# Performance work log

Measured on AMD Instinct MI355X. Metric: run time of the kernel, lower is better.

The kernel has to match this reference:

```python
import jax, jax.numpy as jnp
import numpy as np

HEADS = 4
DIM_HEAD = 64
INNER = HEADS * DIM_HEAD  # 256
MAP_SIZE = (8, 8, 8)
DN = ('NCDHW', 'OIDHW', 'NCDHW')


def _depthwise3d(x, w):
    # x: [B,C,D,H,W], w: [C,1,3,3,3] (torch groups=C layout)
    return jax.lax.conv_general_dilated(
        x, w, window_strides=(1, 1, 1), padding='SAME',
        dimension_numbers=DN, feature_group_count=x.shape[1])


def _dws_conv(x, dw, pw):
    # depthwise 3x3x3 then pointwise 1x1x1 (pw: [out,in])
    y = _depthwise3d(x, dw)
    return jnp.einsum('bcdhw,oc->bodhw', y, pw)


def _split_heads(t):
    # 'b (dim_head heads) d h w -> b heads (d h w) dim_head'
    B, C, D, H, W = t.shape
    t = t.reshape(B, DIM_HEAD, HEADS, D * H * W)
    return t.transpose(0, 2, 3, 1)


def _merge_heads(t, D, H, W):
    # 'b heads n dim_head -> b (dim_head heads) d h w'
    B = t.shape[0]
    return t.transpose(0, 3, 1, 2).reshape(B, DIM_HEAD * HEADS, D, H, W)


def setup_inputs() -> dict:
    key = jax.random.key(0)
    ks = jax.random.split(key, 8)
    B, feat_dim, map_dim, out_dim = 2, 128, 64, 128
    D = H = W = 24
    s = 0.02
    return {
        'feat': jax.random.normal(ks[0], (B, feat_dim, D, H, W), jnp.float32),
        'smap': jax.random.normal(ks[1], (B, map_dim) + MAP_SIZE, jnp.float32),
        'feat_qv_dw': jax.random.normal(ks[2], (feat_dim, 1, 3, 3, 3), jnp.float32) * s,
        'feat_qv_pw': jax.random.normal(ks[3], (2 * INNER, feat_dim), jnp.float32) * s,
        'feat_out_dw': jax.random.normal(ks[4], (INNER, 1, 3, 3, 3), jnp.float32) * s,
        'feat_out_pw': jax.random.normal(ks[5], (out_dim, INNER), jnp.float32) * s,
        'map_qv_w': jax.random.normal(ks[6], (2 * INNER, map_dim), jnp.float32) * s,
        'map_out_w': jax.random.normal(ks[7], (map_dim, INNER), jnp.float32) * s,
    }


def reference(feat, smap, feat_qv_dw, feat_qv_pw, feat_out_dw, feat_out_pw,
              map_qv_w, map_out_w):
    B, C, D, H, W = feat.shape
    scale = DIM_HEAD ** -0.5

    # projections
    fqv = _dws_conv(feat, feat_qv_dw, feat_qv_pw)           # [B, 2*inner, D,H,W]
    feat_q, feat_v = jnp.split(fqv, 2, axis=1)
    mqv = jnp.einsum('bcdhw,oc->bodhw', smap, map_qv_w)     # [B, 2*inner, 8,8,8]
    map_q, map_v = jnp.split(mqv, 2, axis=1)

    feat_q, feat_v = _split_heads(feat_q), _split_heads(feat_v)  # [B,h,N,dh]
    map_q, map_v = _split_heads(map_q), _split_heads(map_v)      # [B,h,M,dh]

    # shared scores, dual-direction softmax
    attn = jnp.einsum('bhid,bhjd->bhij', feat_q, map_q) * scale  # [B,h,N,M]
    feat_map_attn = jax.nn.softmax(attn, axis=-1)
    map_feat_attn = jax.nn.softmax(attn, axis=-2)

    feat_out = jnp.einsum('bhij,bhjd->bhid', feat_map_attn, map_v)   # [B,h,N,dh]
    map_out = jnp.einsum('bhji,bhjd->bhid', map_feat_attn, feat_v)   # [B,h,M,dh]

    feat_out = _merge_heads(feat_out, D, H, W)
    map_out = _merge_heads(map_out, *MAP_SIZE)

    feat_out = _dws_conv(feat_out, feat_out_dw, feat_out_pw)   # [B,out_dim,D,H,W]
    map_out = jnp.einsum('bcdhw,oc->bodhw', map_out, map_out_w)  # [B,map_dim,8,8,8]
    return feat_out, map_out
```

## Files before the change

kernel.cpp:

```cpp
#include <hip/hip_runtime.h>

#define BB 2
#define CH_FEAT 128
#define HEADS 4
#define DH 64
#define INNER 256
#define NPOS 13824
#define MPOS 512
#define DSZ 24
#define JSPLIT 27
#define JCHUNK (NPOS / JSPLIT)

typedef __attribute__((ext_vector_type(8))) short bf16x8;
typedef __attribute__((ext_vector_type(4))) float f32x4;

__device__ inline unsigned short bf16_rn(float x) {
  unsigned u = __builtin_bit_cast(unsigned, x);
  u += 0x7FFF + ((u >> 16) & 1);
  return (unsigned short)(u >> 16);
}
__device__ inline unsigned pk_bf16(float a, float b) {
  return (unsigned)bf16_rn(a) | ((unsigned)bf16_rn(b) << 16);
}
__device__ inline float bf2f(unsigned short u) {
  return __builtin_bit_cast(float, (unsigned)u << 16);
}

#define GL2LDS(g, l)                                                        \
  __builtin_amdgcn_global_load_lds(                                         \
      (const __attribute__((address_space(1))) void*)(g),                   \
      (__attribute__((address_space(3))) void*)(l), 16, 0, 0)

__device__ inline bf16x8 lds_frag(const char* tile, int row, int colb) {
  return *(const bf16x8*)(tile + row * 128 + (colb ^ ((row & 7) << 4)));
}
__device__ inline bf16x8 lds_fragP(const char* tile, int row, int colb, int pitch) {
  return *(const bf16x8*)(tile + row * pitch + (colb ^ ((row & 7) << 4)));
}

__global__ __launch_bounds__(256) void k_pre(const float* __restrict__ smap,
                                             const float* __restrict__ mqv_w,
                                             unsigned short* __restrict__ mapqb,
                                             unsigned short* __restrict__ mapvTb,
                                             const float* __restrict__ feat,
                                             const float* __restrict__ fqv_dw,
                                             unsigned short* __restrict__ dwt) {
  int bid = blockIdx.x;
  int t = threadIdx.x;
  if (bid < 1024) {
    int b = bid >> 9, m = bid & 511;
    __shared__ float s[64];
    if (t < 64) s[t] = smap[(size_t)(b * 64 + t) * MPOS + m];
    __syncthreads();
#pragma unroll
    for (int half = 0; half < 2; ++half) {
      int co2 = half * 256 + t;
      const float* wr = mqv_w + (size_t)co2 * 64;
      float acc = 0.f;
#pragma unroll
      for (int c = 0; c < 64; ++c) acc += wr[c] * s[c];
      int qv = co2 >> 8, c2 = co2 & 255, head = c2 & 3, dh = c2 >> 2;
      int bh = b * HEADS + head;
      if (qv == 0)
        mapqb[((size_t)bh * MPOS + m) * 64 + dh] = bf16_rn(acc * 0.125f);
      else
        mapvTb[((size_t)bh * 64 + dh) * MPOS + m] = bf16_rn(acc);
    }
  } else {
    int tid = (bid - 1024) * 256 + t;
    int bc = tid / 1728;
    int s = tid - bc * 1728;
    int c = bc & (CH_FEAT - 1);
    int xs = (s % 3) * 8;
    int row = s / 3;
    int y = row % 24, z = row / 24;
    const float* wr = fqv_dw + c * 27;
    const float* ip = feat + (size_t)bc * NPOS;

    float w0a[9], w1a[9], w2a[9];
    int ro[9];
#pragma unroll
    for (int dz = 0; dz < 3; ++dz)
#pragma unroll
      for (int dy = 0; dy < 3; ++dy) {
        int r = dz * 3 + dy;
        int zz = z + dz - 1, yy = y + dy - 1;
        bool ok = ((unsigned)zz < 24u) && ((unsigned)yy < 24u);
        w0a[r] = ok ? wr[dz * 9 + dy * 3 + 0] : 0.f;
        w1a[r] = ok ? wr[dz * 9 + dy * 3 + 1] : 0.f;
        w2a[r] = ok ? wr[dz * 9 + dy * 3 + 2] : 0.f;
        int zc = min(max(zz, 0), 23), yc = min(max(yy, 0), 23);
        ro[r] = (zc * 24 + yc) * 24;
      }
    float4 Bv[9], Cv[9];
    float xm1[9], x8[9];
#pragma unroll
    for (int r = 0; r < 9; ++r) {
      Bv[r] = *(const float4*)(ip + ro[r] + xs);
      Cv[r] = *(const float4*)(ip + ro[r] + xs + 4);
      xm1[r] = xs ? *(ip + ro[r] + xs - 1) : 0.f;
      x8[r] = (xs < 16) ? *(ip + ro[r] + xs + 8) : 0.f;
    }
    float acc[8];
#pragma unroll
    for (int i = 0; i < 8; ++i) acc[i] = 0.f;
#pragma unroll
    for (int r = 0; r < 9; ++r) {
      float xv[10] = {xm1[r], Bv[r].x, Bv[r].y, Bv[r].z, Bv[r].w,
                      Cv[r].x, Cv[r].y, Cv[r].z, Cv[r].w, x8[r]};
#pragma unroll
      for (int i = 0; i < 8; ++i)
        acc[i] += w0a[r] * xv[i] + w1a[r] * xv[i + 1] + w2a[r] * xv[i + 2];
    }
    unsigned short* op = dwt + (size_t)bc * NPOS + row * 24 + xs;
    uint4 pv;
    pv.x = pk_bf16(acc[0], acc[1]);
    pv.y = pk_bf16(acc[2], acc[3]);
    pv.z = pk_bf16(acc[4], acc[5]);
    pv.w = pk_bf16(acc[6], acc[7]);
    *(uint4*)op = pv;
  }
}

__global__ __launch_bounds__(256) void k_pwqv_m(const unsigned short* __restrict__ dwt,
                                                const float* __restrict__ pw,
                                                unsigned short* __restrict__ fqb,
                                                unsigned short* __restrict__ fvTb) {
  __shared__ __align__(16) char sW[16384];
  __shared__ __align__(16) char sR[32768];
  __shared__ __align__(16) char sB[32768];
  int t = threadIdx.x, wave = t >> 6, lane = t & 63, g = lane >> 4, c = lane & 15;
  int n0 = blockIdx.x * 128, ti = blockIdx.y, b = blockIdx.z;
  int qv = ti >> 2, head = ti & 3, bh = b * 4 + head;

  {
    int r = t >> 2, ks = (t & 3) * 32;
    int co = qv * 256 + r * 4 + head;
    const float* wp = pw + (size_t)co * 128 + ks;
    unsigned pkv[16];
#pragma unroll
    for (int i = 0; i < 8; ++i) {
      float4 v = *(const float4*)(wp + i * 4);
      pkv[2 * i] = pk_bf16(v.x, v.y);
      pkv[2 * i + 1] = pk_bf16(v.z, v.w);
    }
#pragma unroll
    for (int u = 0; u < 4; ++u) {
      int colb = (ks * 2 + u * 16) ^ ((r & 7) << 4);
      *(uint4*)(sW + r * 256 + colb) = *(uint4*)&pkv[u * 4];
    }
  }
  const char* Bgc = (const char*)(dwt + (size_t)b * CH_FEAT * NPOS);
#pragma unroll
  for (int p = 0; p < 8; ++p) {
    int oo = p * 4096 + t * 16;
    int k = oo >> 8, col = oo & 255;
    GL2LDS(Bgc + (size_t)k * (NPOS * 2) + n0 * 2 + col, sR + oo);
  }
  __syncthreads();

  {
    const unsigned short* R16 = (const unsigned short*)sR;
#pragma unroll
    for (int it = 0; it < 8; ++it) {
      int cid = it * 256 + t;
      int n = cid & 127, kc16 = (cid >> 7) & 15;
      unsigned short v[8];
#pragma unroll
      for (int j = 0; j < 8; ++j) v[j] = R16[(kc16 * 8 + j) * 128 + n];
      unsigned u4[4];
#pragma unroll
      for (int i = 0; i < 4; ++i)
        u4[i] = (unsigned)v[2 * i] | ((unsigned)v[2 * i + 1] << 16);
      *(uint4*)(sB + n * 256 + ((kc16 * 16) ^ ((n & 7) << 4))) = *(uint4*)&u4[0];
    }
  }
  __syncthreads();

  f32x4 acc[4][2];
#pragma unroll
  for (int ct = 0; ct < 4; ++ct)
#pragma unroll
    for (int jf = 0; jf < 2; ++jf) acc[ct][jf] = (f32x4){0.f, 0.f, 0.f, 0.f};
  int nw = wave * 32;
#pragma unroll
  for (int kc = 0; kc < 4; ++kc) {
    bf16x8 bq[2];
#pragma unroll
    for (int jf = 0; jf < 2; ++jf)
      bq[jf] = lds_fragP(sB, nw + jf * 16 + c, kc * 64 + g * 16, 256);
#pragma unroll
    for (int ct = 0; ct < 4; ++ct) {
      bf16x8 a = lds_fragP(sW, ct * 16 + c, kc * 64 + g * 16, 256);
#pragma unroll
      for (int jf = 0; jf < 2; ++jf)
        acc[ct][jf] = __builtin_amdgcn_mfma_f32_16x16x32_bf16(a, bq[jf], acc[ct][jf], 0, 0, 0);
    }
  }
  __syncthreads();

  char* dmp = sR;
#pragma unroll
  for (int ct = 0; ct < 4; ++ct)
#pragma unroll
    for (int jf = 0; jf < 2; ++jf) {
      int n = nw + jf * 16 + c;
      uint2 wv;
      wv.x = pk_bf16(acc[ct][jf][0], acc[ct][jf][1]);
      wv.y = pk_bf16(acc[ct][jf][2], acc[ct][jf][3]);
      *(uint2*)(dmp + n * 144 + (ct * 16 + 4 * g) * 2) = wv;
    }
  __syncthreads();

  if (qv == 0) {
    int nr = t >> 1, seg = t & 1;
    const char* src = dmp + nr * 144 + seg * 64;
    unsigned short* dst = fqb + ((size_t)bh * NPOS + n0 + nr) * 64 + seg * 32;
#pragma unroll
    for (int i = 0; i < 4; ++i)
      *(uint4*)(dst + i * 8) = *(const uint4*)(src + i * 16);
  } else {
#pragma unroll
    for (int it = 0; it < 2; ++it) {
      int idx = it * 256 + t;
      int dh = idx >> 3, nseg = (idx & 7) * 16;
      unsigned pkv[8];
#pragma unroll
      for (int i = 0; i < 8; ++i) {
        unsigned short lo = *(const unsigned short*)(dmp + (nseg + 2 * i) * 144 + dh * 2);
        unsigned short hi = *(const unsigned short*)(dmp + (nseg + 2 * i + 1) * 144 + dh * 2);
        pkv[i] = (unsigned)lo | ((unsigned)hi << 16);
      }
      unsigned short* dst = fvTb + ((size_t)bh * 64 + dh) * NPOS + n0 + nseg;
      *(uint4*)(dst) = *(uint4*)&pkv[0];
      *(uint4*)(dst + 8) = *(uint4*)&pkv[4];
    }
  }
}

__global__ __launch_bounds__(512, 4) void k_attn(const unsigned short* __restrict__ fqb,
                                                 const unsigned short* __restrict__ fvTb,
                                                 const unsigned short* __restrict__ mapqb,
                                                 const unsigned short* __restrict__ mapvTb,
                                                 unsigned short* __restrict__ F,
                                                 float* __restrict__ Gc,
                                                 float* __restrict__ Gl) {
  __shared__ __align__(16) char sAll[70656];
  char* sPool = sAll;
  unsigned (*sP)[2][16][36] = (unsigned (*)[2][16][36])(sAll + 32768);
  float (*sL)[2][16] = (float (*)[2][16])(sAll + 32768 + 36864);
  int bid = blockIdx.x;
  int t = threadIdx.x, wave = t >> 6, lane = t & 63, g = lane >> 4, c = lane & 15;

  if (bid < 432) {
    int jblk = bid % 54, bh = bid / 54;
    int j0 = jblk * 256 + wave * 32;

    const char* Kg = (const char*)(mapqb + (size_t)bh * MPOS * 64);
    const char* Vg = (const char*)(mapvTb + (size_t)bh * 64 * MPOS);

    const unsigned short* fqp = fqb + ((size_t)bh * NPOS + j0 + c) * 64 + 8 * g;
    bf16x8 bq00 = *(const bf16x8*)(fqp);
    bf16x8 bq01 = *(const bf16x8*)(fqp + 32);
    bf16x8 bq10 = *(const bf16x8*)(fqp + 16 * 64);
    bf16x8 bq11 = *(const bf16x8*)(fqp + 16 * 64 + 32);

    f32x4 o[2][4];
#pragma unroll
    for (int jf = 0; jf < 2; ++jf)
#pragma unroll
      for (int dt = 0; dt < 4; ++dt) o[jf][dt] = (f32x4){0.f, 0.f, 0.f, 0.f};
    float ls0 = 0.f, ls1 = 0.f;

    {
      int oo = t * 16;
      int row = oo >> 7, col = (oo & 127) ^ (((oo >> 7) & 7) << 4);
      GL2LDS(Kg + (size_t)row * 128 + col, sPool + oo);
      GL2LDS(Vg + (size_t)row * 1024 + col, sPool + 16384 + oo);
    }
    __syncthreads();

    for (int ic = 0; ic < 8; ++ic) {
      const char* Kt = sPool + (ic & 1) * 8192;
      const char* Vt = sPool + 16384 + (ic & 1) * 8192;
      if (ic < 7) {
        int ibase = (ic + 1) * 64;
        int bsel = ((ic + 1) & 1) * 8192;
        int oo = t * 16;
        int row = oo >> 7, col = (oo & 127) ^ (((oo >> 7) & 7) << 4);
        GL2LDS(Kg + (size_t)(ibase + row) * 128 + col, sPool + bsel + oo);
        GL2LDS(Vg + (size_t)row * 1024 + ibase * 2 + col, sPool + 16384 + bsel + oo);
      }
#pragma unroll
      for (int ti = 0; ti < 4; ++ti) {
        bf16x8 a0 = lds_frag(Kt, ti * 16 + c, 16 * g);
        bf16x8 a1 = lds_frag(Kt, ti * 16 + c, 64 + 16 * g);
        f32x4 s0 = {0.f, 0.f, 0.f, 0.f}, s1 = {0.f, 0.f, 0.f, 0.f};
        s0 = __builtin_amdgcn_mfma_f32_16x16x32_bf16(a0, bq00, s0, 0, 0, 0);
        s0 = __builtin_amdgcn_mfma_f32_16x16x32_bf16(a1, bq01, s0, 0, 0, 0);
        s1 = __builtin_amdgcn_mfma_f32_16x16x32_bf16(a0, bq10, s1, 0, 0, 0);
        s1 = __builtin_amdgcn_mfma_f32_16x16x32_bf16(a1, bq11, s1, 0, 0, 0);
        float p0 = __expf(s0[0]), p1 = __expf(s0[1]), p2 = __expf(s0[2]), p3 = __expf(s0[3]);
        ls0 += (p0 + p1) + (p2 + p3);
        sP[wave][0][c][ti * 8 + 2 * g] = pk_bf16(p0, p1);
        sP[wave][0][c][ti * 8 + 2 * g + 1] = pk_bf16(p2, p3);
        float q0 = __expf(s1[0]), q1 = __expf(s1[1]), q2 = __expf(s1[2]), q3 = __expf(s1[3]);
        ls1 += (q0 + q1) + (q2 + q3);
        sP[wave][1][c][ti * 8 + 2 * g] = pk_bf16(q0, q1);
        sP[wave][1][c][ti * 8 + 2 * g + 1] = pk_bf16(q2, q3);
      }
#pragma unroll
      for (int ks = 0; ks < 2; ++ks) {
        bf16x8 ap0 = *(const bf16x8*)&sP[wave][0][c][ks * 16 + 4 * g];
        bf16x8 ap1 = *(const bf16x8*)&sP[wave][1][c][ks * 16 + 4 * g];
#pragma unroll
        for (int dt = 0; dt < 4; ++dt) {
          bf16x8 bv = lds_frag(Vt, dt * 16 + c, ks * 64 + 16 * g);
          o[0][dt] = __builtin_amdgcn_mfma_f32_16x16x32_bf16(ap0, bv, o[0][dt], 0, 0, 0);
          o[1][dt] = __builtin_amdgcn_mfma_f32_16x16x32_bf16(ap1, bv, o[1][dt], 0, 0, 0);
        }
      }
      __syncthreads();
    }

    ls0 += __shfl_xor(ls0, 16); ls0 += __shfl_xor(ls0, 32);
    ls1 += __shfl_xor(ls1, 16); ls1 += __shfl_xor(ls1, 32);
    if (g == 0) { sL[wave][0][c] = 1.f / ls0; sL[wave][1][c] = 1.f / ls1; }
#pragma unroll
    for (int jf = 0; jf < 2; ++jf) {
      float rl0 = sL[wave][jf][4 * g + 0], rl1 = sL[wave][jf][4 * g + 1];
      float rl2 = sL[wave][jf][4 * g + 2], rl3 = sL[wave][jf][4 * g + 3];
#pragma unroll
      for (int dt = 0; dt < 4; ++dt) {
        uint2 wv;
        wv.x = pk_bf16(o[jf][dt][0] * rl0, o[jf][dt][1] * rl1);
        wv.y = pk_bf16(o[jf][dt][2] * rl2, o[jf][dt][3] * rl3);
        *(uint2*)(sAll + (dt * 16 + c) * 544 + (wave * 32 + jf * 16 + 4 * g) * 2) = wv;
      }
    }
    __syncthreads();
    {
      int ch = t >> 3, seg = t & 7;
      int b = bh >> 2, head = bh & 3;
      unsigned short* dst = F + ((size_t)b * INNER + head * 64 + ch) * NPOS +
                            jblk * 256 + seg * 32;
      const char* src = sAll + ch * 544 + seg * 64;
#pragma unroll
      for (int i = 0; i < 4; ++i)
        *(uint4*)(dst + i * 8) = *(const uint4*)(src + i * 16);
    }
  } else {
    int cid = bid - 432;
    int bh = cid & 7, iblk = (cid >> 3) & 1, chunk = cid >> 4;
    char* sQ = sPool;
    char* sV = sPool + 16384;
    int i0 = iblk * 256 + wave * 32;
    int jb = chunk * JCHUNK;

    const char* Qg = (const char*)(fqb + (size_t)bh * NPOS * 64);
    const char* Vg = (const char*)(fvTb + (size_t)bh * 64 * NPOS);

    const unsigned short* kp = mapqb + ((size_t)bh * MPOS + i0 + c) * 64 + 8 * g;
    bf16x8 bm00 = *(const bf16x8*)(kp);
    bf16x8 bm01 = *(const bf16x8*)(kp + 32);
    bf16x8 bm10 = *(const bf16x8*)(kp + 16 * 64);
    bf16x8 bm11 = *(const bf16x8*)(kp + 16 * 64 + 32);

    f32x4 o[2][4];
#pragma unroll
    for (int f = 0; f < 2; ++f)
#pragma unroll
      for (int dt = 0; dt < 4; ++dt) o[f][dt] = (f32x4){0.f, 0.f, 0.f, 0.f};
    float lc0 = 0.f, lc1 = 0.f;

    {
      int oo = t * 16;
      int row = oo >> 7, col = (oo & 127) ^ (((oo >> 7) & 7) << 4);
      GL2LDS(Qg + (size_t)(jb + row) * 128 + col, sQ + oo);
      GL2LDS(Vg + (size_t)row * (NPOS * 2) + jb * 2 + col, sV + oo);
    }
    __syncthreads();

    for (int jc = 0; jc < JCHUNK / 64; ++jc) {
      const char* Qt = sQ + (jc & 1) * 8192;
      const char* Vt = sV + (jc & 1) * 8192;
      if (jc < JCHUNK / 64 - 1) {
        int jbase = jb + (jc + 1) * 64;
        int bsel = ((jc + 1) & 1) * 8192;
        int oo = t * 16;
        int row = oo >> 7, col = (oo & 127) ^ (((oo >> 7) & 7) << 4);
        GL2LDS(Qg + (size_t)(jbase + row) * 128 + col, sQ + bsel + oo);
        GL2LDS(Vg + (size_t)row * (NPOS * 2) + jbase * 2 + col, sV + bsel + oo);
      }
#pragma unroll
      for (int tj = 0; tj < 4; ++tj) {
        bf16x8 a0 = lds_frag(Qt, tj * 16 + c, 16 * g);
        bf16x8 a1 = lds_frag(Qt, tj * 16 + c, 64 + 16 * g);
        f32x4 s0 = {0.f, 0.f, 0.f, 0.f}, s1 = {0.f, 0.f, 0.f, 0.f};
        s0 = __builtin_amdgcn_mfma_f32_16x16x32_bf16(a0, bm00, s0, 0, 0, 0);
        s0 = __builtin_amdgcn_mfma_f32_16x16x32_bf16(a1, bm01, s0, 0, 0, 0);
        s1 = __builtin_amdgcn_mfma_f32_16x16x32_bf16(a0, bm10, s1, 0, 0, 0);
        s1 = __builtin_amdgcn_mfma_f32_16x16x32_bf16(a1, bm11, s1, 0, 0, 0);
        float p0 = __expf(s0[0]), p1 = __expf(s0[1]), p2 = __expf(s0[2]), p3 = __expf(s0[3]);
        lc0 += (p0 + p1) + (p2 + p3);
        sP[wave][0][c][tj * 8 + 2 * g] = pk_bf16(p0, p1);
        sP[wave][0][c][tj * 8 + 2 * g + 1] = pk_bf16(p2, p3);
        float q0 = __expf(s1[0]), q1 = __expf(s1[1]), q2 = __expf(s1[2]), q3 = __expf(s1[3]);
        lc1 += (q0 + q1) + (q2 + q3);
        sP[wave][1][c][tj * 8 + 2 * g] = pk_bf16(q0, q1);
        sP[wave][1][c][tj * 8 + 2 * g + 1] = pk_bf16(q2, q3);
      }
#pragma unroll
      for (int ks = 0; ks < 2; ++ks) {
        bf16x8 ap0 = *(const bf16x8*)&sP[wave][0][c][ks * 16 + 4 * g];
        bf16x8 ap1 = *(const bf16x8*)&sP[wave][1][c][ks * 16 + 4 * g];
#pragma unroll
        for (int dt = 0; dt < 4; ++dt) {
          bf16x8 bv = lds_frag(Vt, dt * 16 + c, ks * 64 + 16 * g);
          o[0][dt] = __builtin_amdgcn_mfma_f32_16x16x32_bf16(ap0, bv, o[0][dt], 0, 0, 0);
          o[1][dt] = __builtin_amdgcn_mfma_f32_16x16x32_bf16(ap1, bv, o[1][dt], 0, 0, 0);
        }
      }
      __syncthreads();
    }

    lc0 += __shfl_xor(lc0, 16); lc0 += __shfl_xor(lc0, 32);
    lc1 += __shfl_xor(lc1, 16); lc1 += __shfl_xor(lc1, 32);
    int gi = chunk * 8 + bh;
    if (g == 0) {
      Gl[(size_t)gi * MPOS + i0 + c] = lc0;
      Gl[(size_t)gi * MPOS + i0 + 16 + c] = lc1;
    }
    float* gp = Gc + ((size_t)gi * MPOS + i0) * 64;
#pragma unroll
    for (int f = 0; f < 2; ++f)
#pragma unroll
      for (int dt = 0; dt < 4; ++dt)
#pragma unroll
        for (int r = 0; r < 4; ++r)
          gp[(size_t)(f * 16 + 4 * g + r) * 64 + dt * 16 + c] = o[f][dt][r];
  }
}

__global__ __launch_bounds__(256) void k_post(const unsigned short* __restrict__ F,
                                              const float* __restrict__ fout_dw,
                                              unsigned short* __restrict__ dwt2,
                                              const float* __restrict__ Gc,
                                              const float* __restrict__ Gl,
                                              const float* __restrict__ mow,
                                              float* __restrict__ out2) {
  int bid = blockIdx.x;
  int t = threadIdx.x;
  if (bid < 3456) {
    int tid = bid * 256 + t;
    int bc = tid / 1728;
    int s = tid - bc * 1728;
    int c = bc & (INNER - 1), b = bc / INNER;
    int cm = (c & 63) * 4 + (c >> 6);
    int xs = (s % 3) * 8;
    int row = s / 3;
    int y = row % 24, z = row / 24;
    const float* wr = fout_dw + cm * 27;
    const unsigned short* ip = F + (size_t)bc * NPOS;

    float w0a[9], w1a[9], w2a[9];
    int ro[9];
#pragma unroll
    for (int dz = 0; dz < 3; ++dz)
#pragma unroll
      for (int dy = 0; dy < 3; ++dy) {
        int r = dz * 3 + dy;
        int zz = z + dz - 1, yy = y + dy - 1;
        bool ok = ((unsigned)zz < 24u) && ((unsigned)yy < 24u);
        w0a[r] = ok ? wr[dz * 9 + dy * 3 + 0] : 0.f;
        w1a[r] = ok ? wr[dz * 9 + dy * 3 + 1] : 0.f;
        w2a[r] = ok ? wr[dz * 9 + dy * 3 + 2] : 0.f;
        int zc = min(max(zz, 0), 23), yc = min(max(yy, 0), 23);
        ro[r] = (zc * 24 + yc) * 24;
      }
    uint2 Bu[9], Cu[9];
    unsigned short m1[9], p8[9];
#pragma unroll
    for (int r = 0; r < 9; ++r) {
      Bu[r] = *(const uint2*)(ip + ro[r] + xs);
      Cu[r] = *(const uint2*)(ip + ro[r] + xs + 4);
      m1[r] = xs ? ip[ro[r] + xs - 1] : 0;
      p8[r] = (xs < 16) ? ip[ro[r] + xs + 8] : 0;
    }
    float acc[8];
#pragma unroll
    for (int i = 0; i < 8; ++i) acc[i] = 0.f;
#pragma unroll
    for (int r = 0; r < 9; ++r) {
      float xv[10];
      xv[0] = bf2f(m1[r]);
      xv[1] = __builtin_bit_cast(float, (Bu[r].x & 0xFFFFu) << 16);
      xv[2] = __builtin_bit_cast(float, Bu[r].x & 0xFFFF0000u);
      xv[3] = __builtin_bit_cast(float, (Bu[r].y & 0xFFFFu) << 16);
      xv[4] = __builtin_bit_cast(float, Bu[r].y & 0xFFFF0000u);
      xv[5] = __builtin_bit_cast(float, (Cu[r].x & 0xFFFFu) << 16);
      xv[6] = __builtin_bit_cast(float, Cu[r].x & 0xFFFF0000u);
      xv[7] = __builtin_bit_cast(float, (Cu[r].y & 0xFFFFu) << 16);
      xv[8] = __builtin_bit_cast(float, Cu[r].y & 0xFFFF0000u);
      xv[9] = bf2f(p8[r]);
#pragma unroll
      for (int i = 0; i < 8; ++i)
        acc[i] += w0a[r] * xv[i] + w1a[r] * xv[i + 1] + w2a[r] * xv[i + 2];
    }
    unsigned short* op = dwt2 + ((size_t)b * INNER + cm) * NPOS + row * 24 + xs;
    uint4 pv;
    pv.x = pk_bf16(acc[0], acc[1]);
    pv.y = pk_bf16(acc[2], acc[3]);
    pv.z = pk_bf16(acc[4], acc[5]);
    pv.w = pk_bf16(acc[6], acc[7]);
    *(uint4*)op = pv;
  } else {
    int mi = bid - 3456;
    int m = mi & 511, b = mi >> 9;
    __shared__ float sMA[256];
    __shared__ float sL2[4];
    if (t < 4) {
      float l = 0.f;
#pragma unroll 4
      for (int ch = 0; ch < JSPLIT; ++ch)
        l += Gl[(size_t)(ch * 8 + b * 4 + t) * MPOS + m];
      sL2[t] = 1.f / l;
    }
    __syncthreads();
    {
      int head = t & 3, dh = t >> 2;
      int bh = b * 4 + head;
      float a = 0.f;
#pragma unroll 4
      for (int ch = 0; ch < JSPLIT; ++ch)
        a += Gc[((size_t)(ch * 8 + bh) * MPOS + m) * 64 + dh];
      sMA[t] = a * sL2[head];
    }
    __syncthreads();
    if (t < 64) {
      const float* wr = mow + t * 256;
      float acc = 0.f;
#pragma unroll 4
      for (int c = 0; c < 256; ++c) acc += wr[c] * sMA[c];
      out2[((size_t)b * 64 + t) * MPOS + m] = acc;
    }
  }
}

__global__ __launch_bounds__(256) void k_pwout_m(const unsigned short* __restrict__ dwo,
                                                 const float* __restrict__ pw,
                                                 float* __restrict__ out1) {
  __shared__ __align__(16) char sW[32768];
  __shared__ __align__(16) char sB[32768];
  __shared__ __align__(16) char sR[16384];
  int t = threadIdx.x, wave = t >> 6, lane = t & 63, g = lane >> 4, c = lane & 15;
  int n0 = blockIdx.x * 128, ti = blockIdx.y, b = blockIdx.z;

  {
    int r = t >> 2, ks = (t & 3) * 64;
    const float* wp = pw + (size_t)(ti * 64 + r) * 256 + ks;
    unsigned pkv[32];
#pragma unroll
    for (int i = 0; i < 16; ++i) {
      float4 v = *(const float4*)(wp + i * 4);
      pkv[2 * i] = pk_bf16(v.x, v.y);
      pkv[2 * i + 1] = pk_bf16(v.z, v.w);
    }
#pragma unroll
    for (int u = 0; u < 8; ++u) {
      int colb = (ks * 2 + u * 16) ^ ((r & 7) << 4);
      *(uint4*)(sW + r * 512 + colb) = *(uint4*)&pkv[u * 4];
    }
  }

  f32x4 acc[4][2];
#pragma unroll
  for (int ct = 0; ct < 4; ++ct)
#pragma unroll
    for (int jf = 0; jf < 2; ++jf) acc[ct][jf] = (f32x4){0.f, 0.f, 0.f, 0.f};
  int nw = wave * 32;
  const char* Bgc = (const char*)(dwo + (size_t)b * INNER * NPOS);
  const unsigned short* R16 = (const unsigned short*)sR;

  for (int kh = 0; kh < 2; ++kh) {
#pragma unroll
    for (int q = 0; q < 2; ++q) {
#pragma unroll
      for (int p = 0; p < 4; ++p) {
        int oo = p * 4096 + t * 16;
        int kl = oo >> 8, col = oo & 255;
        GL2LDS(Bgc + (size_t)(kh * 128 + q * 64 + kl) * (NPOS * 2) + n0 * 2 + col,
               sR + oo);
      }
      __syncthreads();
#pragma unroll
      for (int it = 0; it < 4; ++it) {
        int cid = it * 256 + t;
        int n = cid & 127, kcl = (cid >> 7) & 7;
        unsigned short v[8];
#pragma unroll
        for (int j = 0; j < 8; ++j) v[j] = R16[(kcl * 8 + j) * 128 + n];
        unsigned u4[4];
#pragma unroll
        for (int i = 0; i < 4; ++i)
          u4[i] = (unsigned)v[2 * i] | ((unsigned)v[2 * i + 1] << 16);
        int kc16 = q * 8 + kcl;
        *(uint4*)(sB + n * 256 + ((kc16 * 16) ^ ((n & 7) << 4))) = *(uint4*)&u4[0];
      }
      __syncthreads();
    }
#pragma unroll
    for (int kc = 0; kc < 4; ++kc) {
      bf16x8 bq[2];
#pragma unroll
      for (int jf = 0; jf < 2; ++jf)
        bq[jf] = lds_fragP(sB, nw + jf * 16 + c, kc * 64 + g * 16, 256);
#pragma unroll
      for (int ct = 0; ct < 4; ++ct) {
        bf16x8 a = lds_fragP(sW, ct * 16 + c, (kh * 4 + kc) * 64 + g * 16, 512);
#pragma unroll
        for (int jf = 0; jf < 2; ++jf)
          acc[ct][jf] = __builtin_amdgcn_mfma_f32_16x16x32_bf16(a, bq[jf], acc[ct][jf], 0, 0, 0);
      }
    }
    __syncthreads();
  }
#pragma unroll
  for (int ct = 0; ct < 4; ++ct)
#pragma unroll
    for (int jf = 0; jf < 2; ++jf) {
      int n = n0 + nw + jf * 16 + c;
#pragma unroll
      for (int r = 0; r < 4; ++r) {
        int co = ti * 64 + ct * 16 + 4 * g + r;
        out1[((size_t)b * 128 + co) * NPOS + n] = acc[ct][jf][r];
      }
    }
}

extern "C" void kernel_launch(void* const* d_in, const int* in_sizes, int n_in,
                              void* d_out, int out_size, void* d_ws, size_t ws_size,
                              hipStream_t stream) {
  const float* feat = (const float*)d_in[0];
  const float* smap = (const float*)d_in[1];
  const float* fqv_dw = (const float*)d_in[2];
  const float* fqv_pw = (const float*)d_in[3];
  const float* fout_dw = (const float*)d_in[4];
  const float* fout_pw = (const float*)d_in[5];
  const float* mqv_w = (const float*)d_in[6];
  const float* mout_w = (const float*)d_in[7];

  float* out = (float*)d_out;
  float* out1 = out;
  float* out2 = out + (size_t)BB * 128 * NPOS;

  const size_t QV = (size_t)BB * HEADS * NPOS * DH;
  const size_t MQV = (size_t)BB * HEADS * MPOS * DH;
  float* ws = (float*)d_ws;
  unsigned short* F = (unsigned short*)ws;
  unsigned short* fqb = (unsigned short*)(ws + QV);
  unsigned short* fvTb = fqb + QV;
  unsigned short* mapqb = fvTb + QV;
  unsigned short* mapvTb = mapqb + MQV;
  float* Gc = (float*)(mapvTb + MQV);
  float* Gl = Gc + (size_t)JSPLIT * 8 * MPOS * 64;

  unsigned short* dwt = (unsigned short*)out1;
  unsigned short* dwt2 = fqb;

  k_pre<<<dim3(1024 + BB * CH_FEAT * 1728 / 256), dim3(256), 0, stream>>>(
      smap, mqv_w, mapqb, mapvTb, feat, fqv_dw, dwt);
  k_pwqv_m<<<dim3(NPOS / 128, 8, BB), dim3(256), 0, stream>>>(dwt, fqv_pw, fqb, fvTb);
  k_attn<<<dim3(432 + 8 * 2 * JSPLIT), dim3(512), 0, stream>>>(
      fqb, fvTb, mapqb, mapvTb, F, Gc, Gl);
  k_post<<<dim3(BB * INNER * 1728 / 256 + BB * MPOS), dim3(256), 0, stream>>>(
      F, fout_dw, dwt2, Gc, Gl, mout_w, out2);
  k_pwout_m<<<dim3(NPOS / 128, 2, BB), dim3(256), 0, stream>>>(dwt2, fout_pw, out1);
}
```

Measured before the change: 177.3 us.

## Fold log2e into map-Q scale, interleave score/PV stages, add MFMA priority

Pre-multiplies the map query scale by log2(e) so the softmax numerators can use the native exp2 instruction instead of expf. Restructures the inner loop to compute scores and apply PV per half-chunk, halving the per-wave P staging buffer and shrinking LDS use so more blocks can reside per CU. Wraps MFMA groups in s_setprio to favour matrix issue. Risks extra LDS hazards between the halves and slightly altered scheduling.

```diff
diff --git a/kernel.cpp b/kernel.cpp
--- a/kernel.cpp
+++ b/kernel.cpp
@@ -10,6 +10,7 @@
 #define DSZ 24
 #define JSPLIT 27
 #define JCHUNK (NPOS / JSPLIT)
+#define QSCALE (0.125f * 1.44269504088896340736f)
 
 typedef __attribute__((ext_vector_type(8))) short bf16x8;
 typedef __attribute__((ext_vector_type(4))) float f32x4;
@@ -62,7 +63,7 @@
       int qv = co2 >> 8, c2 = co2 & 255, head = c2 & 3, dh = c2 >> 2;
       int bh = b * HEADS + head;
       if (qv == 0)
-        mapqb[((size_t)bh * MPOS + m) * 64 + dh] = bf16_rn(acc * 0.125f);
+        mapqb[((size_t)bh * MPOS + m) * 64 + dh] = bf16_rn(acc * QSCALE);
       else
         mapvTb[((size_t)bh * 64 + dh) * MPOS + m] = bf16_rn(acc);
     }
@@ -245,10 +246,10 @@
                                                  unsigned short* __restrict__ F,
                                                  float* __restrict__ Gc,
                                                  float* __restrict__ Gl) {
-  __shared__ __align__(16) char sAll[70656];
+  __shared__ __align__(16) char sAll[52224];
   char* sPool = sAll;
-  unsigned (*sP)[2][16][36] = (unsigned (*)[2][16][36])(sAll + 32768);
-  float (*sL)[2][16] = (float (*)[2][16])(sAll + 32768 + 36864);
+  unsigned (*sP)[2][16][18] = (unsigned (*)[2][16][18])(sAll + 32768);
+  float (*sL)[2][16] = (float (*)[2][16])(sAll + 32768 + 18432);
   int bid = blockIdx.x;
   int t = threadIdx.x, wave = t >> 6, lane = t & 63, g = lane >> 4, c = lane & 15;
 
@@ -292,33 +293,40 @@
         GL2LDS(Vg + (size_t)row * 1024 + ibase * 2 + col, sPool + 16384 + bsel + oo);
       }
 #pragma unroll
-      for (int ti = 0; ti < 4; ++ti) {
-        bf16x8 a0 = lds_frag(Kt, ti * 16 + c, 16 * g);
-        bf16x8 a1 = lds_frag(Kt, ti * 16 + c, 64 + 16 * g);
-        f32x4 s0 = {0.f, 0.f, 0.f, 0.f}, s1 = {0.f, 0.f, 0.f, 0.f};
-        s0 = __builtin_amdgcn_mfma_f32_16x16x32_bf16(a0, bq00, s0, 0, 0, 0);
-        s0 = __builtin_amdgcn_mfma_f32_16x16x32_bf16(a1, bq01, s0, 0, 0, 0);
-        s1 = __builtin_amdgcn_mfma_f32_16x16x32_bf16(a0, bq10, s1, 0, 0, 0);
-        s1 = __builtin_amdgcn_mfma_f32_16x16x32_bf16(a1, bq11, s1, 0, 0, 0);
-        float p0 = __expf(s0[0]), p1 = __expf(s0[1]), p2 = __expf(s0[2]), p3 = __expf(s0[3]);
-        ls0 += (p0 + p1) + (p2 + p3);
-        sP[wave][0][c][ti * 8 + 2 * g] = pk_bf16(p0, p1);
-        sP[wave][0][c][ti * 8 + 2 * g + 1] = pk_bf16(p2, p3);
-        float q0 = __expf(s1[0]), q1 = __expf(s1[1]), q2 = __expf(s1[2]), q3 = __expf(s1[3]);
-        ls1 += (q0 + q1) + (q2 + q3);
-        sP[wave][1][c][ti * 8 + 2 * g] = pk_bf16(q0, q1);
-        sP[wave][1][c][ti * 8 + 2 * g + 1] = pk_bf16(q2, q3);
-      }
-#pragma unroll
       for (int ks = 0; ks < 2; ++ks) {
-        bf16x8 ap0 = *(const bf16x8*)&sP[wave][0][c][ks * 16 + 4 * g];
-        bf16x8 ap1 = *(const bf16x8*)&sP[wave][1][c][ks * 16 + 4 * g];
+#pragma unroll
+        for (int tt = 0; tt < 2; ++tt) {
+          int ti = ks * 2 + tt;
+          bf16x8 a0 = lds_frag(Kt, ti * 16 + c, 16 * g);
+          bf16x8 a1 = lds_frag(Kt, ti * 16 + c, 64 + 16 * g);
+          f32x4 s0 = {0.f, 0.f, 0.f, 0.f}, s1 = {0.f, 0.f, 0.f, 0.f};
+          __builtin_amdgcn_s_setprio(1);
+          s0 = __builtin_amdgcn_mfma_f32_16x16x32_bf16(a0, bq00, s0, 0, 0, 0);
+          s0 = __builtin_amdgcn_mfma_f32_16x16x32_bf16(a1, bq01, s0, 0, 0, 0);
+          s1 = __builtin_amdgcn_mfma_f32_16x16x32_bf16(a0, bq10, s1, 0, 0, 0);
+          s1 = __builtin_amdgcn_mfma_f32_16x16x32_bf16(a1, bq11, s1, 0, 0, 0);
+          __builtin_amdgcn_s_setprio(0);
+          float p0 = __builtin_amdgcn_exp2f(s0[0]), p1 = __builtin_amdgcn_exp2f(s0[1]);
+          float p2 = __builtin_amdgcn_exp2f(s0[2]), p3 = __builtin_amdgcn_exp2f(s0[3]);
+          ls0 += (p0 + p1) + (p2 + p3);
+          sP[wave][0][c][tt * 8 + 2 * g] = pk_bf16(p0, p1);
+          sP[wave][0][c][tt * 8 + 2 * g + 1] = pk_bf16(p2, p3);
+          float q0 = __builtin_amdgcn_exp2f(s1[0]), q1 = __builtin_amdgcn_exp2f(s1[1]);
+          float q2 = __builtin_amdgcn_exp2f(s1[2]), q3 = __builtin_amdgcn_exp2f(s1[3]);
+          ls1 += (q0 + q1) + (q2 + q3);
+          sP[wave][1][c][tt * 8 + 2 * g] = pk_bf16(q0, q1);
+          sP[wave][1][c][tt * 8 + 2 * g + 1] = pk_bf16(q2, q3);
+        }
+        bf16x8 ap0 = *(const bf16x8*)&sP[wave][0][c][4 * g];
+        bf16x8 ap1 = *(const bf16x8*)&sP[wave][1][c][4 * g];
+        __builtin_amdgcn_s_setprio(1);
 #pragma unroll
         for (int dt = 0; dt < 4; ++dt) {
           bf16x8 bv = lds_frag(Vt, dt * 16 + c, ks * 64 + 16 * g);
           o[0][dt] = __builtin_amdgcn_mfma_f32_16x16x32_bf16(ap0, bv, o[0][dt], 0, 0, 0);
           o[1][dt] = __builtin_amdgcn_mfma_f32_16x16x32_bf16(ap1, bv, o[1][dt], 0, 0, 0);
         }
+        __builtin_amdgcn_s_setprio(0);
       }
       __syncthreads();
     }
@@ -393,33 +401,40 @@
         GL2LDS(Vg + (size_t)row * (NPOS * 2) + jbase * 2 + col, sV + bsel + oo);
       }
 #pragma unroll
-      for (int tj = 0; tj < 4; ++tj) {
-        bf16x8 a0 = lds_frag(Qt, tj * 16 + c, 16 * g);
-        bf16x8 a1 = lds_frag(Qt, tj * 16 + c, 64 + 16 * g);
-        f32x4 s0 = {0.f, 0.f, 0.f, 0.f}, s1 = {0.f, 0.f, 0.f, 0.f};
-        s0 = __builtin_amdgcn_mfma_f32_16x16x32_bf16(a0, bm00, s0, 0, 0, 0);
-        s0 = __builtin_amdgcn_mfma_f32_16x16x32_bf16(a1, bm01, s0, 0, 0, 0);
-        s1 = __builtin_amdgcn_mfma_f32_16x16x32_bf16(a0, bm10, s1, 0, 0, 0);
-        s1 = __builtin_amdgcn_mfma_f32_16x16x32_bf16(a1, bm11, s1, 0, 0, 0);
-        float p0 = __expf(s0[0]), p1 = __expf(s0[1]), p2 = __expf(s0[2]), p3 = __expf(s0[3]);
-        lc0 += (p0 + p1) + (p2 + p3);
-        sP[wave][0][c][tj * 8 + 2 * g] = pk_bf16(p0, p1);
-        sP[wave][0][c][tj * 8 + 2 * g + 1] = pk_bf16(p2, p3);
-        float q0 = __expf(s1[0]), q1 = __expf(s1[1]), q2 = __expf(s1[2]), q3 = __expf(s1[3]);
-        lc1 += (q0 + q1) + (q2 + q3);
-        sP[wave][1][c][tj * 8 + 2 * g] = pk_bf16(q0, q1);
-        sP[wave][1][c][tj * 8 + 2 * g + 1] = pk_bf16(q2, q3);
-      }
-#pragma unroll
       for (int ks = 0; ks < 2; ++ks) {
-        bf16x8 ap0 = *(const bf16x8*)&sP[wave][0][c][ks * 16 + 4 * g];
-        bf16x8 ap1 = *(const bf16x8*)&sP[wave][1][c][ks * 16 + 4 * g];
+#pragma unroll
+        for (int tt = 0; tt < 2; ++tt) {
+          int tj = ks * 2 + tt;
+          bf16x8 a0 = lds_frag(Qt, tj * 16 + c, 16 * g);
+          bf16x8 a1 = lds_frag(Qt, tj * 16 + c, 64 + 16 * g);
+          f32x4 s0 = {0.f, 0.f, 0.f, 0.f}, s1 = {0.f, 0.f, 0.f, 0.f};
+          __builtin_amdgcn_s_setprio(1);
+          s0 = __builtin_amdgcn_mfma_f32_16x16x32_bf16(a0, bm00, s0, 0, 0, 0);
+          s0 = __builtin_amdgcn_mfma_f32_16x16x32_bf16(a1, bm01, s0, 0, 0, 0);
+          s1 = __builtin_amdgcn_mfma_f32_16x16x32_bf16(a0, bm10, s1, 0, 0, 0);
+          s1 = __builtin_amdgcn_mfma_f32_16x16x32_bf16(a1, bm11, s1, 0, 0, 0);
+          __builtin_amdgcn_s_setprio(0);
+          float p0 = __builtin_amdgcn_exp2f(s0[0]), p1 = __builtin_amdgcn_exp2f(s0[1]);
+          float p2 = __builtin_amdgcn_exp2f(s0[2]), p3 = __builtin_amdgcn_exp2f(s0[3]);
+          lc0 += (p0 + p1) + (p2 + p3);
+          sP[wave][0][c][tt * 8 + 2 * g] = pk_bf16(p0, p1);
+          sP[wave][0][c][tt * 8 + 2 * g + 1] = pk_bf16(p2, p3);
+          float q0 = __builtin_amdgcn_exp2f(s1[0]), q1 = __builtin_amdgcn_exp2f(s1[1]);
+          float q2 = __builtin_amdgcn_exp2f(s1[2]), q3 = __builtin_amdgcn_exp2f(s1[3]);
+          lc1 += (q0 + q1) + (q2 + q3);
+          sP[wave][1][c][tt * 8 + 2 * g] = pk_bf16(q0, q1);
+          sP[wave][1][c][tt * 8 + 2 * g + 1] = pk_bf16(q2, q3);
+        }
+        bf16x8 ap0 = *(const bf16x8*)&sP[wave][0][c][4 * g];
+        bf16x8 ap1 = *(const bf16x8*)&sP[wave][1][c][4 * g];
+        __builtin_amdgcn_s_setprio(1);
 #pragma unroll
         for (int dt = 0; dt < 4; ++dt) {
           bf16x8 bv = lds_frag(Vt, dt * 16 + c, ks * 64 + 16 * g);
           o[0][dt] = __builtin_amdgcn_mfma_f32_16x16x32_bf16(ap0, bv, o[0][dt], 0, 0, 0);
           o[1][dt] = __builtin_amdgcn_mfma_f32_16x16x32_bf16(ap1, bv, o[1][dt], 0, 0, 0);
         }
+        __builtin_amdgcn_s_setprio(0);
       }
       __syncthreads();
     }
```

Result: slower. 190.0 us (+7.1%).
